# Performance work log

Hardware: AMD Instinct MI355X
Metric: run time of the kernel (lower is better)

Reference implementation:

```python
import jax, jax.numpy as jnp
import numpy as np

B, S, D = 4, 2048, 512
H, HD, RL = 8, 64, 64   # nheads, head_dim = D//H, rl_dim
TEMPER = 1.0
BETA = 1.0
SLOPE = 0.01  # LeakyReLU negative slope
LN_EPS = 1e-5


def setup_inputs() -> dict:
    key = jax.random.key(0)
    ks = jax.random.split(key, 12)
    scale = 0.02
    return {
        "h":   jax.random.normal(ks[0], (B, S, D), dtype=jnp.float32),
        "rh":  jax.random.normal(ks[1], (B, S, RL), dtype=jnp.float32),
        "Wl":  jax.random.normal(ks[2], (D, D), dtype=jnp.float32) * scale,   # linear_l (in,out)
        "Wr":  jax.random.normal(ks[3], (D, D), dtype=jnp.float32) * scale,   # linear_r
        "al":  jax.random.normal(ks[4], (HD,), dtype=jnp.float32) * scale,    # att_l: Linear(head_dim,1)
        "ar":  jax.random.normal(ks[5], (HD,), dtype=jnp.float32) * scale,    # att_r
        "Wrs": jax.random.normal(ks[6], (RL, RL * H), dtype=jnp.float32) * scale,  # r_source
        "Wrt": jax.random.normal(ks[7], (RL, RL * H), dtype=jnp.float32) * scale,  # r_target
        "Wf":  jax.random.normal(ks[8], (D, D), dtype=jnp.float32) * scale,   # linear_final
        "ln_g": jnp.ones((D,), dtype=jnp.float32),
        "ln_b": jnp.zeros((D,), dtype=jnp.float32),
    }


def _layer_norm(x, g, b):
    mu = jnp.mean(x, axis=-1, keepdims=True)
    var = jnp.mean(jnp.square(x - mu), axis=-1, keepdims=True)
    return (x - mu) * jax.lax.rsqrt(var + LN_EPS) * g + b


def reference(h, rh, Wl, Wr, al, ar, Wrs, Wrt, Wf, ln_g, ln_b):
    leaky = lambda x: jnp.where(x >= 0, x, SLOPE * x)
    # projections -> [B, H, S, HD]
    fl = (h @ Wl).reshape(B, S, H, HD).transpose(0, 2, 1, 3)
    fr = (h @ Wr).reshape(B, S, H, HD).transpose(0, 2, 1, 3)
    # additive attention logits: [B,H,S,1] + [B,H,1,S]
    sl = jnp.einsum('bhsd,d->bhs', leaky(fl), al)
    sr = jnp.einsum('bhsd,d->bhs', leaky(fr), ar)
    score = sl[:, :, :, None] + sr[:, :, None, :]
    # relation-embedding bilinear bias: r_k @ r_q -> [B,H,S,S]
    r_k = (rh @ Wrs).reshape(B, S, H, RL).transpose(0, 2, 1, 3)   # [B,H,S,RL]
    r_q = (rh @ Wrt).reshape(B, S, H, RL).transpose(0, 2, 3, 1)   # [B,H,RL,S]
    score = score + BETA * jnp.einsum('bhsr,bhrt->bhst', r_k, r_q)
    score = jax.nn.softmax(score / TEMPER, axis=-1)
    # context and output projection (dropout = 0 -> identity)
    context = jnp.einsum('bhst,bhtd->bhsd', score, fr)
    h_sa = context.transpose(0, 2, 1, 3).reshape(B, S, H * HD)
    fh = h_sa @ Wf
    return _layer_norm(h + fh, ln_g, ln_b)
```

## Files before the change

### kernel.cpp

```cpp
#include <hip/hip_runtime.h>
#include <math.h>

#define B_ 4
#define S_ 2048
#define D_ 512
#define H_ 8
#define HD_ 64
#define RL_ 64
#define LN_EPS 1e-5f
#define SLOPE 0.01f
#define LOG2E 1.4426950408889634f

typedef __attribute__((ext_vector_type(8))) __bf16 bf16x8;
typedef __attribute__((ext_vector_type(4))) float f32x4;
typedef __attribute__((ext_vector_type(16))) float f32x16;

__device__ __forceinline__ float leaky(float x) { return x >= 0.f ? x : SLOPE * x; }

__device__ __forceinline__ ushort f2bf(float f) {
    union { float f; unsigned u; } v; v.f = f;
    unsigned r = v.u + 0x7fffu + ((v.u >> 16) & 1u);
    return (ushort)(r >> 16);
}
__device__ __forceinline__ unsigned cvtpk(float a, float b) {
    unsigned r;
    asm("v_cvt_pk_bf16_f32 %0, %1, %2" : "=v"(r) : "v"(a), "v"(b));
    return r;
}

__device__ __forceinline__ void g2lds16(const void* g, void* l) {
    __builtin_amdgcn_global_load_lds(
        (const __attribute__((address_space(1))) void*)(uintptr_t)g,
        (__attribute__((address_space(3))) void*)(uintptr_t)l, 16, 0, 0);
}

__device__ __forceinline__ void plane32swap(unsigned &x, unsigned &y) {
    asm volatile("v_permlane32_swap_b32 %0, %1" : "+v"(x), "+v"(y));
}

__global__ __launch_bounds__(256) void prep(
    const float* __restrict__ h, const float* __restrict__ rh,
    const float* __restrict__ Wr, const float* __restrict__ Wf,
    const float* __restrict__ Wrs, const float* __restrict__ Wrt,
    ushort* __restrict__ hb, ushort* __restrict__ rhb,
    ushort* __restrict__ WrT, ushort* __restrict__ WfT,
    ushort* __restrict__ WrsT, ushort* __restrict__ WrtT)
{
    const int bx = blockIdx.x, tid = threadIdx.x;
    if (bx < 4608) {
        const float* in = (bx < 4096) ? h : rh;
        ushort* o = (bx < 4096) ? hb : rhb;
        const int i = (bx < 4096 ? bx : bx - 4096) * 256 + tid;
        const float4 v = ((const float4*)in)[i];
        ushort4 u; u.x = f2bf(v.x); u.y = f2bf(v.y); u.z = f2bf(v.z); u.w = f2bf(v.w);
        ((ushort4*)o)[i] = u;
        return;
    }
    __shared__ float TS[64][65];
    int t = bx - 4608;
    const float* in; ushort* out; int K, tk, tn;
    if (t < 64)       { in = Wr;  out = WrT;  K = 512; tk = t & 7; tn = t >> 3; }
    else if (t < 128) { in = Wf;  out = WfT;  K = 512; t -= 64; tk = t & 7; tn = t >> 3; }
    else if (t < 136) { in = Wrs; out = WrsT; K = 64;  tk = 0; tn = t - 128; }
    else              { in = Wrt; out = WrtT; K = 64;  tk = 0; tn = t - 136; }
    const int k0 = tk * 64, n0 = tn * 64;
    const int r = tid >> 4, c4 = (tid & 15) * 4;
    #pragma unroll
    for (int p = 0; p < 4; ++p) {
        const int row = r + 16 * p;
        const float4 v = *(const float4*)(in + (size_t)(k0 + row) * 512 + n0 + c4);
        TS[row][c4] = v.x; TS[row][c4 + 1] = v.y;
        TS[row][c4 + 2] = v.z; TS[row][c4 + 3] = v.w;
    }
    __syncthreads();
    #pragma unroll
    for (int p = 0; p < 4; ++p) {
        const int nn = r + 16 * p;
        ushort4 o;
        o.x = f2bf(TS[c4 + 0][nn]); o.y = f2bf(TS[c4 + 1][nn]);
        o.z = f2bf(TS[c4 + 2][nn]); o.w = f2bf(TS[c4 + 3][nn]);
        *(ushort4*)(out + (size_t)(n0 + nn) * K + k0 + c4) = o;
    }
}

__global__ __launch_bounds__(256) void proj(
    const ushort* __restrict__ hb, const ushort* __restrict__ rhb,
    const ushort* __restrict__ WrT, const ushort* __restrict__ WrsT,
    const ushort* __restrict__ WrtT,
    ushort* __restrict__ frT, ushort* __restrict__ rkw, ushort* __restrict__ rqw,
    float* __restrict__ sred, const float* __restrict__ ar)
{
    __shared__ ushort As[2][64 * 32];
    __shared__ ushort Bs[2][128 * 32];

    const int tid = threadIdx.x;
    const int lane = tid & 63, w = tid >> 6;
    const int ln = lane & 15, quad = lane >> 4;
    const int wm = w >> 1, wn = w & 1;
    const int m0 = blockIdx.x * 64, n0 = blockIdx.y * 128;
    const int z = blockIdx.z;

    const ushort* A; const ushort* wt; ushort* co; float scl; int K;
    if (z == 0)      { A = hb;  wt = WrT;  co = frT; scl = LOG2E; K = 512; }
    else if (z == 1) { A = rhb; wt = WrsT; co = rkw; scl = LOG2E; K = 64; }
    else             { A = rhb; wt = WrtT; co = rqw; scl = 1.0f;  K = 64; }

    const int srA = tid >> 2;
    const int lchA = ((lane & 3) - (srA >> 1)) & 3;
    const ushort* AgB = A + (size_t)(m0 + srA) * K + lchA * 8;
    const int srB = w * 32 + (lane >> 2);
    const int lchB = ((lane & 3) - (srB >> 1)) & 3;
    const ushort* BgB0 = wt + (size_t)(n0 + srB) * K + lchB * 8;
    const ushort* BgB1 = BgB0 + (size_t)16 * K;
    const int aoff = tid * 8;
    const int boff = srB * 32 + (lane & 3) * 8;
    const int pc = (quad + (ln >> 1)) & 3;

    g2lds16(AgB, &As[0][aoff]);
    g2lds16(BgB0, &Bs[0][boff]);
    g2lds16(BgB1, &Bs[0][boff + 512]);

    f32x4 acc[2][4] = {};
    int buf = 0;
    for (int k0 = 0; k0 < K; k0 += 32) {
        __syncthreads();
        if (k0 + 32 < K) {
            g2lds16(AgB + k0 + 32, &As[buf ^ 1][aoff]);
            g2lds16(BgB0 + k0 + 32, &Bs[buf ^ 1][boff]);
            g2lds16(BgB1 + k0 + 32, &Bs[buf ^ 1][boff + 512]);
        }
        bf16x8 af[2], bfr[4];
        #pragma unroll
        for (int mi = 0; mi < 2; ++mi)
            af[mi] = *(const bf16x8*)&As[buf][(wm * 32 + mi * 16 + ln) * 32 + pc * 8];
        #pragma unroll
        for (int ni = 0; ni < 4; ++ni)
            bfr[ni] = *(const bf16x8*)&Bs[buf][(wn * 64 + ni * 16 + ln) * 32 + pc * 8];
        #pragma unroll
        for (int mi = 0; mi < 2; ++mi)
            #pragma unroll
            for (int ni = 0; ni < 4; ++ni)
                acc[mi][ni] = __builtin_amdgcn_mfma_f32_16x16x32_bf16(
                    af[mi], bfr[ni], acc[mi][ni], 0, 0, 0);
        buf ^= 1;
    }

    const int head = blockIdx.y * 2 + wn;
    const int b = m0 >> 11;
    const size_t bh = (size_t)b * H_ + head;
    if (z == 0) {
        #pragma unroll
        for (int mi = 0; mi < 2; ++mi) {
            const int s = (m0 & (S_ - 1)) + wm * 32 + mi * 16 + quad * 4;
            const int sp = (s & ~15) | ((((0x1320u >> (quad * 4)) & 0xFu)) << 2);
            #pragma unroll
            for (int ni = 0; ni < 4; ++ni) {
                const int d = ni * 16 + ln;
                ushort4 o;
                o.x = f2bf(acc[mi][ni][0]); o.y = f2bf(acc[mi][ni][1]);
                o.z = f2bf(acc[mi][ni][2]); o.w = f2bf(acc[mi][ni][3]);
                *(ushort4*)(co + (bh * 64 + d) * S_ + sp) = o;
            }
        }
        float a4[4];
        #pragma unroll
        for (int ni = 0; ni < 4; ++ni) a4[ni] = ar[ni * 16 + ln];
        #pragma unroll
        for (int mi = 0; mi < 2; ++mi) {
            const int s = (m0 & (S_ - 1)) + wm * 32 + mi * 16 + quad * 4;
            #pragma unroll
            for (int r = 0; r < 4; ++r) {
                float v = 0.f;
                #pragma unroll
                for (int ni = 0; ni < 4; ++ni)
                    v += leaky(acc[mi][ni][r]) * a4[ni];
                #pragma unroll
                for (int off = 8; off; off >>= 1) v += __shfl_xor(v, off, 16);
                if (ln == 0) sred[bh * S_ + s + r] = v * scl;
            }
        }
    } else {
        #pragma unroll
        for (int mi = 0; mi < 2; ++mi) {
            const int s = (m0 & (S_ - 1)) + wm * 32 + mi * 16 + quad * 4;
            #pragma unroll
            for (int ni = 0; ni < 4; ++ni) {
                const int d = ni * 16 + ln;
                #pragma unroll
                for (int r = 0; r < 4; ++r)
                    co[(bh * S_ + s + r) * 64 + d] = f2bf(acc[mi][ni][r] * scl);
            }
        }
    }
}

#define WAITV(N) asm volatile("s_waitcnt vmcnt(" #N ")" ::: "memory")
#define BARR()   __builtin_amdgcn_s_barrier()

__global__ __launch_bounds__(256, 1) void attn_mfma(
    const ushort* __restrict__ frT, const ushort* __restrict__ rk,
    const ushort* __restrict__ rq, const float* __restrict__ sr,
    ushort* __restrict__ hsa)
{
    __shared__ ushort SMEM[16384];
    __shared__ float  LS[4][2][64];
    ushort* RQp = SMEM;
    ushort* FTp = SMEM + 8192;

    const int tid = threadIdx.x;
    const int w = tid >> 6;
    const int qg = w >> 1;
    const int th = w & 1;
    const int lane = tid & 63;
    const int lq = lane & 31;
    const int hi = lane >> 5;

    const int flat = blockIdx.x + 16 * (blockIdx.y + 8 * blockIdx.z);
    const int wid = (flat & 7) * 64 + (flat >> 3);
    const int q0 = (wid & 15) * 128;
    const int h = (wid >> 4) & 7;
    const int b = wid >> 7;
    const size_t bh = (size_t)b * H_ + h;
    const int qb = q0 + 64 * qg;

    bf16x8 bq[2][4];
    #pragma unroll
    for (int qt = 0; qt < 2; ++qt) {
        const ushort* p = rk + ((bh * S_ + qb + 32 * qt + lq) << 6) + hi * 8;
        #pragma unroll
        for (int ks = 0; ks < 4; ++ks)
            bq[qt][ks] = *(const bf16x8*)(p + ks * 16);
    }

    const ushort* rq_g = rq + (bh * S_ << 6);
    const ushort* ft_g = frT + (size_t)bh * 64 * S_;
    const float* srp = sr + bh * S_;

    const int srow = tid >> 3;
    const int pg = tid & 7;
    const int oS = (pg - (srow & 7)) & 7;

    #define STAGE(BUF, t0)                                                    \
        { _Pragma("unroll")                                                   \
          for (int j = 0; j < 2; ++j) {                                       \
            const int rr = 32 * j + srow;                                     \
            g2lds16(rq_g + ((size_t)((t0) + rr) << 6) + oS * 8,               \
                    RQp + (BUF) * 4096 + rr * 64 + pg * 8);                   \
            g2lds16(ft_g + (size_t)rr * S_ + (t0) + oS * 8,                   \
                    FTp + (BUF) * 4096 + rr * 64 + pg * 8);                   \
          } }

    f32x16 ctx[2][2] = {};
    float lsum[2] = {0.f, 0.f};

    #define COMPUTE(BI, TC)                                                    \
    {                                                                          \
        bf16x8 af[4];                                                          \
        _Pragma("unroll")                                                      \
        for (int ks = 0; ks < 4; ++ks)                                         \
            af[ks] = *(const bf16x8*)(RQp + (BI) * 4096 + (th * 32 + lq) * 64  \
                       + ((2 * ks + hi + (lq & 7)) & 7) * 8);                  \
        f32x16 s0 = {}; f32x16 s1 = {};                                        \
        _Pragma("unroll")                                                      \
        for (int ks = 0; ks < 4; ++ks) {                                       \
            s0 = __builtin_amdgcn_mfma_f32_32x32x16_bf16(af[ks], bq[0][ks], s0, 0, 0, 0); \
            s1 = __builtin_amdgcn_mfma_f32_32x32x16_bf16(af[ks], bq[1][ks], s1, 0, 0, 0); \
        }                                                                      \
        float sva[16];                                                         \
        _Pragma("unroll")                                                      \
        for (int jj = 0; jj < 4; ++jj) {                                       \
            const float4 v = *(const float4*)(srp + (TC) + th * 32 + jj * 8 + hi * 4); \
            sva[jj * 4 + 0] = v.x; sva[jj * 4 + 1] = v.y;                      \
            sva[jj * 4 + 2] = v.z; sva[jj * 4 + 3] = v.w;                      \
        }                                                                      \
        uint4 paw[2][2];                                                       \
        _Pragma("unroll")                                                      \
        for (int qt = 0; qt < 2; ++qt) {                                       \
            float p[16];                                                       \
            _Pragma("unroll")                                                  \
            for (int r = 0; r < 16; ++r)                                       \
                p[r] = __builtin_amdgcn_exp2f((qt ? s1[r] : s0[r]) + sva[r]);  \
            float ls = 0.f;                                                    \
            _Pragma("unroll")                                                  \
            for (int r = 0; r < 16; ++r) ls += p[r];                           \
            lsum[qt] += ls;                                                    \
            _Pragma("unroll")                                                  \
            for (int c = 0; c < 2; ++c) {                                      \
                const int e = 8 * c;                                           \
                unsigned c01 = cvtpk(p[e + 0], p[e + 1]);                      \
                unsigned c23 = cvtpk(p[e + 2], p[e + 3]);                      \
                unsigned c45 = cvtpk(p[e + 4], p[e + 5]);                      \
                unsigned c67 = cvtpk(p[e + 6], p[e + 7]);                      \
                plane32swap(c45, c67);                                         \
                paw[qt][c] = make_uint4(c01, c23, c67, c45);                   \
            }                                                                  \
        }                                                                      \
        _Pragma("unroll")                                                      \
        for (int c = 0; c < 2; ++c) {                                          \
            _Pragma("unroll")                                                  \
            for (int dt = 0; dt < 2; ++dt) {                                   \
                const bf16x8 fv = *(const bf16x8*)(FTp + (BI) * 4096           \
                    + (dt * 32 + lq) * 64                                      \
                    + ((4 * th + 2 * c + hi + (lq & 7)) & 7) * 8);             \
                ctx[0][dt] = __builtin_amdgcn_mfma_f32_32x32x16_bf16(          \
                    __builtin_bit_cast(bf16x8, paw[0][c]), fv, ctx[0][dt], 0, 0, 0); \
                ctx[1][dt] = __builtin_amdgcn_mfma_f32_32x32x16_bf16(          \
                    __builtin_bit_cast(bf16x8, paw[1][c]), fv, ctx[1][dt], 0, 0, 0); \
            }                                                                  \
        }                                                                      \
    }

    STAGE(0, 0)
    for (int it = 0; it < 15; ++it) {
        const int t0 = it * 128;
        WAITV(0); BARR();
        STAGE(1, t0 + 64)
        COMPUTE(0, t0)
        WAITV(0); BARR();
        STAGE(0, t0 + 128)
        COMPUTE(1, t0 + 64)
    }
    WAITV(0); BARR();
    STAGE(1, 1984)
    COMPUTE(0, 1920)
    WAITV(0); BARR();
    COMPUTE(1, 1984)

    BARR();
    float* CX = (float*)SMEM;
    float* CXw = CX + w * 2048;

    #define EPILOGUE(OWN, OTH)                                                \
    {                                                                         \
        _Pragma("unroll")                                                     \
        for (int qt = 0; qt < 2; ++qt)                                        \
            _Pragma("unroll")                                                 \
            for (int r = 0; r < 16; ++r)                                      \
                CXw[(qt * 16 + r) * 64 + lane] = ctx[qt][OTH][r];             \
        LS[w][0][lane] = lsum[0];                                             \
        LS[w][1][lane] = lsum[1];                                             \
        BARR();                                                               \
        const float* CXp = CX + (w ^ 1) * 2048;                               \
        _Pragma("unroll")                                                     \
        for (int qt = 0; qt < 2; ++qt) {                                      \
            float lt = lsum[qt] + LS[w ^ 1][qt][lane];                        \
            const float l = lt + __shfl_xor(lt, 32, 64);                      \
            const float inv = 1.f / l;                                        \
            _Pragma("unroll")                                                 \
            for (int r = 0; r < 16; ++r) {                                    \
                const float cv = ctx[qt][OWN][r] + CXp[(qt * 16 + r) * 64 + lane]; \
                const int rho = (r & 3) + 8 * (r >> 2) + 4 * hi;              \
                const float fi = __shfl(inv, rho, 64);                        \
                const int q = qb + 32 * qt + rho;                             \
                hsa[(size_t)(b * S_ + q) * D_ + h * 64 + (OWN) * 32 + lq] = f2bf(cv * fi); \
            }                                                                 \
        }                                                                     \
    }

    if (th == 0) EPILOGUE(0, 1)
    else         EPILOGUE(1, 0)
}

__global__ __launch_bounds__(256) void gemm_out(
    const ushort* __restrict__ A, const ushort* __restrict__ WT,
    float* __restrict__ C)
{
    __shared__ ushort As[2][64 * 32];
    __shared__ ushort Bs[2][128 * 32];

    const int tid = threadIdx.x;
    const int lane = tid & 63, w = tid >> 6;
    const int ln = lane & 15, quad = lane >> 4;
    const int wm = w >> 1, wn = w & 1;
    const int m0 = blockIdx.x * 64, n0 = blockIdx.y * 128;
    const int K = 512;

    const int srA = tid >> 2;
    const int lchA = ((lane & 3) - (srA >> 1)) & 3;
    const ushort* AgB = A + (size_t)(m0 + srA) * K + lchA * 8;
    const int srB = w * 32 + (lane >> 2);
    const int lchB = ((lane & 3) - (srB >> 1)) & 3;
    const ushort* BgB0 = WT + (size_t)(n0 + srB) * K + lchB * 8;
    const ushort* BgB1 = BgB0 + (size_t)16 * K;
    const int aoff = tid * 8;
    const int boff = srB * 32 + (lane & 3) * 8;
    const int pc = (quad + (ln >> 1)) & 3;

    g2lds16(AgB, &As[0][aoff]);
    g2lds16(BgB0, &Bs[0][boff]);
    g2lds16(BgB1, &Bs[0][boff + 512]);

    f32x4 acc[2][4] = {};
    int buf = 0;
    for (int k0 = 0; k0 < K; k0 += 32) {
        __syncthreads();
        if (k0 + 32 < K) {
            g2lds16(AgB + k0 + 32, &As[buf ^ 1][aoff]);
            g2lds16(BgB0 + k0 + 32, &Bs[buf ^ 1][boff]);
            g2lds16(BgB1 + k0 + 32, &Bs[buf ^ 1][boff + 512]);
        }
        bf16x8 af[2], bfr[4];
        #pragma unroll
        for (int mi = 0; mi < 2; ++mi)
            af[mi] = *(const bf16x8*)&As[buf][(wm * 32 + mi * 16 + ln) * 32 + pc * 8];
        #pragma unroll
        for (int ni = 0; ni < 4; ++ni)
            bfr[ni] = *(const bf16x8*)&Bs[buf][(wn * 64 + ni * 16 + ln) * 32 + pc * 8];
        #pragma unroll
        for (int mi = 0; mi < 2; ++mi)
            #pragma unroll
            for (int ni = 0; ni < 4; ++ni)
                acc[mi][ni] = __builtin_amdgcn_mfma_f32_16x16x32_bf16(
                    af[mi], bfr[ni], acc[mi][ni], 0, 0, 0);
        buf ^= 1;
    }

    #pragma unroll
    for (int mi = 0; mi < 2; ++mi) {
        const int row = m0 + wm * 32 + mi * 16 + quad * 4;
        #pragma unroll
        for (int ni = 0; ni < 4; ++ni) {
            const int col = n0 + wn * 64 + ni * 16 + ln;
            #pragma unroll
            for (int r = 0; r < 4; ++r)
                C[(size_t)(row + r) * 512 + col] = acc[mi][ni][r];
        }
    }
}

__global__ __launch_bounds__(256) void ln_kernel(
    const float* __restrict__ h, const float* __restrict__ fh,
    const float* __restrict__ g, const float* __restrict__ bb,
    float* __restrict__ out)
{
    const int row = blockIdx.x, tid = threadIdx.x;
    const float* hp = h + (size_t)row * 512;
    const float* fp = fh + (size_t)row * 512;
    const float x0 = hp[tid] + fp[tid];
    const float x1 = hp[tid + 256] + fp[tid + 256];
    __shared__ float red[4];

    float s = x0 + x1;
    #pragma unroll
    for (int off = 32; off; off >>= 1) s += __shfl_xor(s, off, 64);
    if ((tid & 63) == 0) red[tid >> 6] = s;
    __syncthreads();
    const float mu = (red[0] + red[1] + red[2] + red[3]) * (1.f / 512.f);

    const float d0 = x0 - mu, d1 = x1 - mu;
    float v = d0 * d0 + d1 * d1;
    #pragma unroll
    for (int off = 32; off; off >>= 1) v += __shfl_xor(v, off, 64);
    __syncthreads();
    if ((tid & 63) == 0) red[tid >> 6] = v;
    __syncthreads();
    const float var = (red[0] + red[1] + red[2] + red[3]) * (1.f / 512.f);
    const float inv = rsqrtf(var + LN_EPS);

    out[(size_t)row * 512 + tid] = d0 * inv * g[tid] + bb[tid];
    out[(size_t)row * 512 + tid + 256] = d1 * inv * g[tid + 256] + bb[tid + 256];
}

extern "C" void kernel_launch(void* const* d_in, const int* in_sizes, int n_in,
                              void* d_out, int out_size, void* d_ws, size_t ws_size,
                              hipStream_t stream)
{
    const float* h   = (const float*)d_in[0];
    const float* rh  = (const float*)d_in[1];
    const float* Wr  = (const float*)d_in[3];
    const float* ar  = (const float*)d_in[5];
    const float* Wrs = (const float*)d_in[6];
    const float* Wrt = (const float*)d_in[7];
    const float* Wf  = (const float*)d_in[8];
    const float* lng = (const float*)d_in[9];
    const float* lnb = (const float*)d_in[10];
    float* out = (float*)d_out;
    char* wsb  = (char*)d_ws;

    const size_t MB = (size_t)1 << 20;
    ushort* hb   = (ushort*)(wsb);
    ushort* rhb  = (ushort*)(wsb + 8 * MB);
    ushort* WrT  = (ushort*)(wsb + 9 * MB);
    ushort* WfT  = (ushort*)(wsb + 9 * MB + 512 * 1024);
    ushort* WrsT = (ushort*)(wsb + 10 * MB);
    ushort* WrtT = (ushort*)(wsb + 10 * MB + 64 * 1024);
    ushort* frT  = (ushort*)(wsb + 11 * MB);
    ushort* rkw  = (ushort*)(wsb + 19 * MB);
    ushort* rqw  = (ushort*)(wsb + 27 * MB);
    float*  sr   = (float*) (wsb + 35 * MB);
    ushort* hsab = (ushort*)(wsb + 36 * MB);
    float*  fh   = (float*) (wsb + 44 * MB);

    dim3 blk(256);
    prep<<<dim3(4752), blk, 0, stream>>>(h, rh, Wr, Wf, Wrs, Wrt,
                                         hb, rhb, WrT, WfT, WrsT, WrtT);
    proj<<<dim3(128, 4, 3), blk, 0, stream>>>(hb, rhb, WrT, WrsT, WrtT,
                                              frT, rkw, rqw, sr, ar);
    attn_mfma<<<dim3(S_ / 128, H_, B_), blk, 0, stream>>>(frT, rkw, rqw, sr, hsab);
    gemm_out<<<dim3(128, 4), blk, 0, stream>>>(hsab, WfT, fh);
    ln_kernel<<<dim3(B_ * S_), blk, 0, stream>>>(h, fh, lng, lnb, out);
}
```

Measured before the change: 174.3 us.

## Fuse output projection GEMM with residual add and LayerNorm

Replaces the separate output GEMM and LayerNorm kernels with one kernel. Each block now computes a full 32-row by 512-column tile, so the residual add and the row mean and variance are done in registers with cross-wave reductions through shared memory. This removes the fp32 fh intermediate round trip through global memory and one kernel launch. In exchange the launch shrinks to 256 larger blocks at occupancy 1, each streaming the whole weight matrix, which lowers parallelism and adds weight reload traffic.

```diff
diff --git a/kernel.cpp b/kernel.cpp
--- a/kernel.cpp
+++ b/kernel.cpp
@@ -361,104 +361,131 @@
     else         EPILOGUE(1, 0)
 }
 
-__global__ __launch_bounds__(256) void gemm_out(
+__global__ __launch_bounds__(256, 1) void gemm_ln(
     const ushort* __restrict__ A, const ushort* __restrict__ WT,
-    float* __restrict__ C)
+    const float* __restrict__ hres, const float* __restrict__ g,
+    const float* __restrict__ bb, float* __restrict__ out)
 {
-    __shared__ ushort As[2][64 * 32];
-    __shared__ ushort Bs[2][128 * 32];
+    __shared__ ushort As[2][32 * 32];
+    __shared__ ushort Bs[2][512 * 32];
+    __shared__ float  RS[32][4];
 
     const int tid = threadIdx.x;
     const int lane = tid & 63, w = tid >> 6;
     const int ln = lane & 15, quad = lane >> 4;
-    const int wm = w >> 1, wn = w & 1;
-    const int m0 = blockIdx.x * 64, n0 = blockIdx.y * 128;
     const int K = 512;
+
+    const int blk = (blockIdx.x & 7) * 32 + (blockIdx.x >> 3);
+    const int m0 = blk * 32;
 
     const int srA = tid >> 2;
     const int lchA = ((lane & 3) - (srA >> 1)) & 3;
     const ushort* AgB = A + (size_t)(m0 + srA) * K + lchA * 8;
-    const int srB = w * 32 + (lane >> 2);
-    const int lchB = ((lane & 3) - (srB >> 1)) & 3;
-    const ushort* BgB0 = WT + (size_t)(n0 + srB) * K + lchB * 8;
-    const ushort* BgB1 = BgB0 + (size_t)16 * K;
     const int aoff = tid * 8;
-    const int boff = srB * 32 + (lane & 3) * 8;
+
+    const int rb = 128 * w + (lane >> 2);
+
+    f32x4 acc[2][8] = {};
+
+    if (tid < 128) g2lds16(AgB, &As[0][aoff]);
+    #pragma unroll
+    for (int j = 0; j < 8; ++j) {
+        const int rw = rb + 16 * j;
+        const int lchB = ((lane & 3) - (rw >> 1)) & 3;
+        g2lds16(WT + (size_t)rw * K + lchB * 8, &Bs[0][rw * 32 + (lane & 3) * 8]);
+    }
+
     const int pc = (quad + (ln >> 1)) & 3;
-
-    g2lds16(AgB, &As[0][aoff]);
-    g2lds16(BgB0, &Bs[0][boff]);
-    g2lds16(BgB1, &Bs[0][boff + 512]);
-
-    f32x4 acc[2][4] = {};
     int buf = 0;
     for (int k0 = 0; k0 < K; k0 += 32) {
         __syncthreads();
         if (k0 + 32 < K) {
-            g2lds16(AgB + k0 + 32, &As[buf ^ 1][aoff]);
-            g2lds16(BgB0 + k0 + 32, &Bs[buf ^ 1][boff]);
-            g2lds16(BgB1 + k0 + 32, &Bs[buf ^ 1][boff + 512]);
-        }
-        bf16x8 af[2], bfr[4];
+            if (tid < 128) g2lds16(AgB + k0 + 32, &As[buf ^ 1][aoff]);
+            #pragma unroll
+            for (int j = 0; j < 8; ++j) {
+                const int rw = rb + 16 * j;
+                const int lchB = ((lane & 3) - (rw >> 1)) & 3;
+                g2lds16(WT + (size_t)rw * K + k0 + 32 + lchB * 8,
+                        &Bs[buf ^ 1][rw * 32 + (lane & 3) * 8]);
+            }
+        }
+        bf16x8 af[2], bfr[8];
         #pragma unroll
         for (int mi = 0; mi < 2; ++mi)
-            af[mi] = *(const bf16x8*)&As[buf][(wm * 32 + mi * 16 + ln) * 32 + pc * 8];
-        #pragma unroll
-        for (int ni = 0; ni < 4; ++ni)
-            bfr[ni] = *(const bf16x8*)&Bs[buf][(wn * 64 + ni * 16 + ln) * 32 + pc * 8];
+            af[mi] = *(const bf16x8*)&As[buf][(mi * 16 + ln) * 32 + pc * 8];
+        #pragma unroll
+        for (int ni = 0; ni < 8; ++ni)
+            bfr[ni] = *(const bf16x8*)&Bs[buf][(w * 128 + ni * 16 + ln) * 32 + pc * 8];
         #pragma unroll
         for (int mi = 0; mi < 2; ++mi)
             #pragma unroll
-            for (int ni = 0; ni < 4; ++ni)
+            for (int ni = 0; ni < 8; ++ni)
                 acc[mi][ni] = __builtin_amdgcn_mfma_f32_16x16x32_bf16(
                     af[mi], bfr[ni], acc[mi][ni], 0, 0, 0);
         buf ^= 1;
     }
 
-    #pragma unroll
-    for (int mi = 0; mi < 2; ++mi) {
-        const int row = m0 + wm * 32 + mi * 16 + quad * 4;
-        #pragma unroll
-        for (int ni = 0; ni < 4; ++ni) {
-            const int col = n0 + wn * 64 + ni * 16 + ln;
-            #pragma unroll
-            for (int r = 0; r < 4; ++r)
-                C[(size_t)(row + r) * 512 + col] = acc[mi][ni][r];
-        }
-    }
-}
-
-__global__ __launch_bounds__(256) void ln_kernel(
-    const float* __restrict__ h, const float* __restrict__ fh,
-    const float* __restrict__ g, const float* __restrict__ bb,
-    float* __restrict__ out)
-{
-    const int row = blockIdx.x, tid = threadIdx.x;
-    const float* hp = h + (size_t)row * 512;
-    const float* fp = fh + (size_t)row * 512;
-    const float x0 = hp[tid] + fp[tid];
-    const float x1 = hp[tid + 256] + fp[tid + 256];
-    __shared__ float red[4];
-
-    float s = x0 + x1;
-    #pragma unroll
-    for (int off = 32; off; off >>= 1) s += __shfl_xor(s, off, 64);
-    if ((tid & 63) == 0) red[tid >> 6] = s;
+    float gg[8], bv[8];
+    #pragma unroll
+    for (int ni = 0; ni < 8; ++ni) {
+        const int col = 128 * w + ni * 16 + ln;
+        gg[ni] = g[col]; bv[ni] = bb[col];
+    }
+
+    #pragma unroll
+    for (int mi = 0; mi < 2; ++mi)
+        #pragma unroll
+        for (int r = 0; r < 4; ++r) {
+            const int rl = mi * 16 + quad * 4 + r;
+            const float* hp = hres + (size_t)(m0 + rl) * 512 + 128 * w + ln;
+            float s = 0.f;
+            #pragma unroll
+            for (int ni = 0; ni < 8; ++ni) {
+                acc[mi][ni][r] += hp[ni * 16];
+                s += acc[mi][ni][r];
+            }
+            #pragma unroll
+            for (int off = 8; off; off >>= 1) s += __shfl_xor(s, off, 16);
+            if (ln == 0) RS[rl][w] = s;
+        }
     __syncthreads();
-    const float mu = (red[0] + red[1] + red[2] + red[3]) * (1.f / 512.f);
-
-    const float d0 = x0 - mu, d1 = x1 - mu;
-    float v = d0 * d0 + d1 * d1;
-    #pragma unroll
-    for (int off = 32; off; off >>= 1) v += __shfl_xor(v, off, 64);
+    float mu[2][4];
+    #pragma unroll
+    for (int mi = 0; mi < 2; ++mi)
+        #pragma unroll
+        for (int r = 0; r < 4; ++r) {
+            const int rl = mi * 16 + quad * 4 + r;
+            mu[mi][r] = (RS[rl][0] + RS[rl][1] + RS[rl][2] + RS[rl][3]) * (1.f / 512.f);
+        }
     __syncthreads();
-    if ((tid & 63) == 0) red[tid >> 6] = v;
+    #pragma unroll
+    for (int mi = 0; mi < 2; ++mi)
+        #pragma unroll
+        for (int r = 0; r < 4; ++r) {
+            const int rl = mi * 16 + quad * 4 + r;
+            float v = 0.f;
+            #pragma unroll
+            for (int ni = 0; ni < 8; ++ni) {
+                const float d = acc[mi][ni][r] - mu[mi][r];
+                v += d * d;
+            }
+            #pragma unroll
+            for (int off = 8; off; off >>= 1) v += __shfl_xor(v, off, 16);
+            if (ln == 0) RS[rl][w] = v;
+        }
     __syncthreads();
-    const float var = (red[0] + red[1] + red[2] + red[3]) * (1.f / 512.f);
-    const float inv = rsqrtf(var + LN_EPS);
-
-    out[(size_t)row * 512 + tid] = d0 * inv * g[tid] + bb[tid];
-    out[(size_t)row * 512 + tid + 256] = d1 * inv * g[tid + 256] + bb[tid + 256];
+    #pragma unroll
+    for (int mi = 0; mi < 2; ++mi)
+        #pragma unroll
+        for (int r = 0; r < 4; ++r) {
+            const int rl = mi * 16 + quad * 4 + r;
+            const float var = (RS[rl][0] + RS[rl][1] + RS[rl][2] + RS[rl][3]) * (1.f / 512.f);
+            const float inv = rsqrtf(var + LN_EPS);
+            float* op = out + (size_t)(m0 + rl) * 512 + 128 * w + ln;
+            #pragma unroll
+            for (int ni = 0; ni < 8; ++ni)
+                op[ni * 16] = (acc[mi][ni][r] - mu[mi][r]) * inv * gg[ni] + bv[ni];
+        }
 }
 
 extern "C" void kernel_launch(void* const* d_in, const int* in_sizes, int n_in,
@@ -489,7 +516,6 @@
     ushort* rqw  = (ushort*)(wsb + 27 * MB);
     float*  sr   = (float*) (wsb + 35 * MB);
     ushort* hsab = (ushort*)(wsb + 36 * MB);
-    float*  fh   = (float*) (wsb + 44 * MB);
 
     dim3 blk(256);
     prep<<<dim3(4752), blk, 0, stream>>>(h, rh, Wr, Wf, Wrs, Wrt,
@@ -497,6 +523,5 @@
     proj<<<dim3(128, 4, 3), blk, 0, stream>>>(hb, rhb, WrT, WrsT, WrtT,
                                               frT, rkw, rqw, sr, ar);
     attn_mfma<<<dim3(S_ / 128, H_, B_), blk, 0, stream>>>(frT, rkw, rqw, sr, hsab);
-    gemm_out<<<dim3(128, 4), blk, 0, stream>>>(hsab, WfT, fh);
-    ln_kernel<<<dim3(B_ * S_), blk, 0, stream>>>(h, fh, lng, lnb, out);
-}
+    gemm_ln<<<dim3(256), blk, 0, stream>>>(hsab, WfT, h, lng, lnb, out);
+}
```

New measurement: 177.7 us. No clear change (+2.0%).
